# Optimization experiments

Hardware: AMD Instinct MI355X
Metric: run time of the kernel (lower is better)

## Reference

```python
import jax, jax.numpy as jnp
import numpy as np

B, LH, HF = 65536, 128, 32
VC_MIN = 0.0


def _theta_init():
    # Deterministic parameter init, matching the torch constructor defaults.
    def spinv(x):
        return float(np.log(np.exp(max(x, 1e-4)) - 1.0 + 1e-6))
    vals = [
        0.0,                                  # alpha_raw: log(0.5/(1-0.5))
        float(np.log(np.exp(1.0) - 1.0 + 1e-6)),   # c_raw  (c_init=1.0)
        float(np.log(np.exp(0.1) - 1.0 + 1e-6)),   # kappa_raw (kappa_init=0.1)
        float(np.log(np.exp(0.15) - 1.0 + 1e-6)),  # vc_raw (vc_eff=0.15)
        -6.0,   # log_qx
        -6.0,   # log_qu
        -5.0,   # log_r
        0.0,    # log_q_scale
        -6.0,   # log_p0_xx
        -4.0,   # log_p0_uu
        spinv(0.1),   # a1_raw
        spinv(0.05),  # d1_raw
        spinv(0.5),   # d2_raw
        spinv(0.5),   # d3_raw
        0.0,    # b1
        0.0,    # b2
        0.1,    # beta
        float(np.arctanh(0.9)),  # rho_m_raw
        -4.0,   # log_qm
        -4.0,   # log_p0_mm
    ]
    return np.asarray(vals, dtype=np.float32)


def setup_inputs() -> dict:
    key = jax.random.key(0)
    k1, k2, k3, k4, k5 = jax.random.split(key, 5)
    return {
        "v_hist": jax.random.normal(k1, (B, LH), dtype=jnp.float32),
        "dt_hist": 0.01 + 0.1 * jax.random.uniform(k2, (B, LH), dtype=jnp.float32),
        "x_obs_hist": jax.random.normal(k3, (B, LH), dtype=jnp.float32),
        "v_fut": jax.random.normal(k4, (B, HF), dtype=jnp.float32),
        "dt_fut": 0.01 + 0.1 * jax.random.uniform(k5, (B, HF), dtype=jnp.float32),
        "theta": jnp.asarray(_theta_init()),
    }


def _forward(v_hist, dt_hist, x_obs_hist, v_fut, dt_fut, theta):
    sp = jax.nn.softplus
    alpha = jax.nn.sigmoid(theta[0])
    c = sp(theta[1]); kappa = sp(theta[2]); vc = sp(theta[3]) + VC_MIN
    qx = jnp.exp(theta[4]); qu = jnp.exp(theta[5]); R = jnp.exp(theta[6])
    qs = jnp.exp(theta[7]); p0xx = jnp.exp(theta[8]); p0uu = jnp.exp(theta[9])
    a1 = sp(theta[10]); d1 = sp(theta[11]); d2 = sp(theta[12]); d3 = sp(theta[13])
    b1 = theta[14]; b2 = theta[15]; beta = theta[16]
    rho_m = jnp.tanh(theta[17]); qm = jnp.exp(theta[18]); p0mm = jnp.exp(theta[19])

    Bn, Lh = v_hist.shape
    dtype = v_hist.dtype
    eye = jnp.eye(3, dtype=dtype)

    def predict(s, P, v, dv, dt):
        x, u, m = s[:, 0], s[:, 1], s[:, 2]
        rho = jnp.exp(-alpha * dt)
        forcing = jax.nn.relu(v * v - vc * vc)
        cl = (-a1 * u + b1 * v + b2 * dv
              - d1 * u * u - d2 * u * jnp.abs(v) - d3 * u * jnp.abs(u))
        x_p = x + u * dt
        u_p = rho * u - kappa * x * dt + c * forcing * dt + cl * dt + beta * m
        m_p = rho_m * m
        s_p = jnp.stack([x_p, u_p, m_p], axis=1)
        z = jnp.zeros_like(dt); o = jnp.ones_like(dt)
        Fm = jnp.stack([
            jnp.stack([o, dt, z], axis=1),
            jnp.stack([-kappa * dt, rho, beta * o], axis=1),
            jnp.stack([z, z, rho_m * o], axis=1)], axis=1)  # [B,3,3]
        qdiag = jnp.stack([qs * qx * dt, qs * qu * dt, qm * o], axis=1)  # [B,3]
        P_p = jnp.einsum('bij,bjk,blk->bil', Fm, P, Fm) + qdiag[:, :, None] * eye
        return s_p, P_p

    def update(s, P, y):
        innov = y - s[:, 0]
        S = P[:, 0, 0] + R
        K = P[:, :, 0] / S[:, None]            # [B,3]
        s_u = s + K * innov[:, None]
        IKH = eye - K[:, :, None] * eye[0]     # I - K H, H = [1,0,0]
        P_u = (jnp.einsum('bij,bjk,blk->bil', IKH, P, IKH)
               + R * (K[:, :, None] * K[:, None, :]))
        return s_u, P_u

    s0 = jnp.zeros((Bn, 3), dtype).at[:, 0].set(x_obs_hist[:, 0])
    P0 = jnp.broadcast_to(jnp.diag(jnp.stack([p0xx, p0uu, p0mm])).astype(dtype),
                          (Bn, 3, 3))

    # History steps k = 1 .. Lh-1 (scan over time axis, [T, B] layout)
    v_h = v_hist[:, :Lh - 1].T
    dv_h = jnp.concatenate(
        [jnp.zeros((1, Bn), dtype), (v_hist[:, 1:Lh - 1] - v_hist[:, :Lh - 2]).T], axis=0)
    dt_h = jnp.maximum(dt_hist[:, 1:], 1e-6).T
    y_h = x_obs_hist[:, 1:].T

    def hist_step(carry, inp):
        s, P = carry
        v, dv, dt, y = inp
        s, P = predict(s, P, v, dv, dt)
        s, P = update(s, P, y)
        return (s, P), None

    (s, P), _ = jax.lax.scan(hist_step, (s0, P0), (v_h, dv_h, dt_h, y_h))

    # Future rollout (predict only)
    v_f = v_fut.T
    dv_f = (v_fut - jnp.concatenate([v_hist[:, -1:], v_fut[:, :-1]], axis=1)).T
    dt_f = jnp.maximum(dt_fut, 1e-6).T

    def fut_step(carry, inp):
        s, P = carry
        v, dv, dt = inp
        s, P = predict(s, P, v, dv, dt)
        return (s, P), (s[:, 0], P[:, 0, 0], s[:, 1])

    _, (x_preds, x_vars, u_ests) = jax.lax.scan(fut_step, (s, P), (v_f, dv_f, dt_f))
    return x_preds.T, x_vars.T, u_ests.T  # each [B, Hf]


def reference(v_hist, dt_hist, x_obs_hist, v_fut, dt_fut, theta):
    return _forward(v_hist, dt_hist, x_obs_hist, v_fut, dt_fut, theta)
```

## Files before the change

kernel.cpp:

```cpp
#include <hip/hip_runtime.h>
#include <math.h>

#define BATCH 65536
#define LHIST 128
#define HFUT  32

__device__ __forceinline__ float softplusf(float x) {
    return fmaxf(x, 0.0f) + log1pf(expf(-fabsf(x)));
}

__global__ __launch_bounds__(256, 1) void kalman_fwd(
    const float* __restrict__ v_hist,
    const float* __restrict__ dt_hist,
    const float* __restrict__ x_obs,
    const float* __restrict__ v_fut,
    const float* __restrict__ dt_fut,
    const float* __restrict__ theta,
    float* __restrict__ out)
{
    const int b = blockIdx.x * 256 + threadIdx.x;

    const float alpha = 1.0f / (1.0f + expf(-theta[0]));
    const float c     = softplusf(theta[1]);
    const float kappa = softplusf(theta[2]);
    const float vc    = softplusf(theta[3]);
    const float qx    = expf(theta[4]);
    const float qu    = expf(theta[5]);
    const float Rn    = expf(theta[6]);
    const float qs    = expf(theta[7]);
    const float p0xx  = expf(theta[8]);
    const float p0uu  = expf(theta[9]);
    const float a1    = softplusf(theta[10]);
    const float d1    = softplusf(theta[11]);
    const float d2    = softplusf(theta[12]);
    const float d3    = softplusf(theta[13]);
    const float b1    = theta[14];
    const float b2    = theta[15];
    const float beta  = theta[16];
    const float rho_m = tanhf(theta[17]);
    const float qm    = expf(theta[18]);
    const float p0mm  = expf(theta[19]);
    const float vc2   = vc * vc;
    const float qxs   = qs * qx;
    const float qus   = qs * qu;
    const float nal2e = -alpha * 1.44269504088896340736f;

    float sx = 0.0f, su = 0.0f, sm = 0.0f;
    float p00 = p0xx, p01 = 0.0f, p02 = 0.0f, p11 = p0uu, p12 = 0.0f, p22 = p0mm;

    auto predict = [&](float v, float dv, float dt_raw) {
        float dt  = fmaxf(dt_raw, 1e-6f);
        float rho = __builtin_amdgcn_exp2f(nal2e * dt);
        float forcing = fmaxf(v * v - vc2, 0.0f);
        float cl = -a1 * su + b1 * v + b2 * dv
                 - d1 * su * su - d2 * su * fabsf(v) - d3 * su * fabsf(su);
        float kdt = kappa * dt;
        float x_p = sx + su * dt;
        float u_p = rho * su - kdt * sx + c * forcing * dt + cl * dt + beta * sm;
        float m_p = rho_m * sm;
        float f0 = p00 + dt * p01;
        float f1 = p01 + dt * p11;
        float f2 = p02 + dt * p12;
        float g0 = -kdt * p00 + rho * p01 + beta * p02;
        float g1 = -kdt * p01 + rho * p11 + beta * p12;
        float g2 = -kdt * p02 + rho * p12 + beta * p22;
        float n00 = f0 + dt * f1 + qxs * dt;
        float n01 = -kdt * f0 + rho * f1 + beta * f2;
        float n02 = rho_m * f2;
        float n11 = -kdt * g0 + rho * g1 + beta * g2 + qus * dt;
        float n12 = rho_m * g2;
        float n22 = rho_m * rho_m * p22 + qm;
        sx = x_p; su = u_p; sm = m_p;
        p00 = n00; p01 = n01; p02 = n02; p11 = n11; p12 = n12; p22 = n22;
    };

    auto update = [&](float y) {
        float innov = y - sx;
        float S    = p00 + Rn;
        float Sinv = __builtin_amdgcn_rcpf(S);
        float K0 = p00 * Sinv, K1 = p01 * Sinv, K2 = p02 * Sinv;
        sx += K0 * innov; su += K1 * innov; sm += K2 * innov;
        float a = 1.0f - K0;
        float n00 = a * a * p00 + Rn * K0 * K0;
        float n01 = a * (p01 - K1 * p00) + Rn * K0 * K1;
        float n02 = a * (p02 - K2 * p00) + Rn * K0 * K2;
        float n11 = S * K1 * K1 - 2.0f * K1 * p01 + p11;
        float n12 = S * K1 * K2 - K2 * p01 - K1 * p02 + p12;
        float n22 = S * K2 * K2 - 2.0f * K2 * p02 + p22;
        p00 = n00; p01 = n01; p02 = n02; p11 = n11; p12 = n12; p22 = n22;
    };

    const float4* v4 = (const float4*)(v_hist  + (size_t)b * LHIST);
    const float4* d4 = (const float4*)(dt_hist + (size_t)b * LHIST);
    const float4* y4 = (const float4*)(x_obs   + (size_t)b * LHIST);

    float4 AV0, AV1, AV2, AV3, AD0, AD1, AD2, AD3, AY0, AY1, AY2, AY3;
    float4 BV0, BV1, BV2, BV3, BD0, BD1, BD2, BD3, BY0, BY1, BY2, BY3;
    float vp1 = 0.0f, vp2 = 0.0f;

#define LOAD_CHUNK(k, P) do {                                                    \
    P##V0 = v4[4*(k)+0]; P##V1 = v4[4*(k)+1];                                    \
    P##V2 = v4[4*(k)+2]; P##V3 = v4[4*(k)+3];                                    \
    P##D0 = d4[4*(k)+0]; P##D1 = d4[4*(k)+1];                                    \
    P##D2 = d4[4*(k)+2]; P##D3 = d4[4*(k)+3];                                    \
    P##Y0 = y4[4*(k)+0]; P##Y1 = y4[4*(k)+1];                                    \
    P##Y2 = y4[4*(k)+2]; P##Y3 = y4[4*(k)+3];                                    \
} while (0)

#define KSTEP(vc_, vpv_, dtn_, yn_) do { predict((vc_), (vc_) - (vpv_), (dtn_)); update(yn_); } while (0)

#define CHUNK_TAIL(P) do {                                                       \
    KSTEP(P##V0.y, P##V0.x, P##D0.z, P##Y0.z);                                   \
    KSTEP(P##V0.z, P##V0.y, P##D0.w, P##Y0.w);                                   \
    KSTEP(P##V0.w, P##V0.z, P##D1.x, P##Y1.x);                                   \
    KSTEP(P##V1.x, P##V0.w, P##D1.y, P##Y1.y);                                   \
    KSTEP(P##V1.y, P##V1.x, P##D1.z, P##Y1.z);                                   \
    KSTEP(P##V1.z, P##V1.y, P##D1.w, P##Y1.w);                                   \
    KSTEP(P##V1.w, P##V1.z, P##D2.x, P##Y2.x);                                   \
    KSTEP(P##V2.x, P##V1.w, P##D2.y, P##Y2.y);                                   \
    KSTEP(P##V2.y, P##V2.x, P##D2.z, P##Y2.z);                                   \
    KSTEP(P##V2.z, P##V2.y, P##D2.w, P##Y2.w);                                   \
    KSTEP(P##V2.w, P##V2.z, P##D3.x, P##Y3.x);                                   \
    KSTEP(P##V3.x, P##V2.w, P##D3.y, P##Y3.y);                                   \
    KSTEP(P##V3.y, P##V3.x, P##D3.z, P##Y3.z);                                   \
    KSTEP(P##V3.z, P##V3.y, P##D3.w, P##Y3.w);                                   \
    vp2 = P##V3.z; vp1 = P##V3.w;                                                \
} while (0)

#define CHUNK(P) do {                                                            \
    predict(vp1, vp1 - vp2, P##D0.x);   update(P##Y0.x);                         \
    KSTEP(P##V0.x, vp1, P##D0.y, P##Y0.y);                                       \
    CHUNK_TAIL(P);                                                               \
} while (0)

    LOAD_CHUNK(0, A);
    LOAD_CHUNK(1, B);

    sx = AY0.x;
    predict(AV0.x, 0.0f, AD0.y); update(AY0.y);
    CHUNK_TAIL(A);

    #pragma unroll 1
    for (int k = 1; k <= 3; ++k) {
        LOAD_CHUNK(2 * k, A);
        CHUNK(B);
        LOAD_CHUNK(2 * k + 1, B);
        CHUNK(A);
    }

    const float4* vf4 = (const float4*)(v_fut  + (size_t)b * HFUT);
    const float4* df4 = (const float4*)(dt_fut + (size_t)b * HFUT);
    float4 VF0 = vf4[0], VF1 = vf4[1], VF2 = vf4[2], VF3 = vf4[3],
           VF4 = vf4[4], VF5 = vf4[5], VF6 = vf4[6], VF7 = vf4[7];
    float4 DF0 = df4[0], DF1 = df4[1], DF2 = df4[2], DF3 = df4[3],
           DF4 = df4[4], DF5 = df4[5], DF6 = df4[6], DF7 = df4[7];

    CHUNK(B);

    float4 OP0, OP1, OP2, OP3, OP4, OP5, OP6, OP7;
    float4 OV0, OV1, OV2, OV3, OV4, OV5, OV6, OV7;
    float4 OU0, OU1, OU2, OU3, OU4, OU5, OU6, OU7;
    float vp = vp1;

#define FUTQ(VF, DF, OP, OV, OU) do {                                            \
    predict(VF.x, VF.x - vp,   DF.x); OP.x = sx; OV.x = p00; OU.x = su;          \
    predict(VF.y, VF.y - VF.x, DF.y); OP.y = sx; OV.y = p00; OU.y = su;          \
    predict(VF.z, VF.z - VF.y, DF.z); OP.z = sx; OV.z = p00; OU.z = su;          \
    predict(VF.w, VF.w - VF.z, DF.w); OP.w = sx; OV.w = p00; OU.w = su;          \
    vp = VF.w;                                                                   \
} while (0)

    FUTQ(VF0, DF0, OP0, OV0, OU0);
    FUTQ(VF1, DF1, OP1, OV1, OU1);
    FUTQ(VF2, DF2, OP2, OV2, OU2);
    FUTQ(VF3, DF3, OP3, OV3, OU3);
    FUTQ(VF4, DF4, OP4, OV4, OU4);
    FUTQ(VF5, DF5, OP5, OV5, OU5);
    FUTQ(VF6, DF6, OP6, OV6, OU6);
    FUTQ(VF7, DF7, OP7, OV7, OU7);

    float4* xp = (float4*)(out + (size_t)b * HFUT);
    float4* xv = (float4*)(out + (size_t)BATCH * HFUT + (size_t)b * HFUT);
    float4* ue = (float4*)(out + 2 * (size_t)BATCH * HFUT + (size_t)b * HFUT);
    xp[0] = OP0; xp[1] = OP1; xp[2] = OP2; xp[3] = OP3;
    xp[4] = OP4; xp[5] = OP5; xp[6] = OP6; xp[7] = OP7;
    xv[0] = OV0; xv[1] = OV1; xv[2] = OV2; xv[3] = OV3;
    xv[4] = OV4; xv[5] = OV5; xv[6] = OV6; xv[7] = OV7;
    ue[0] = OU0; ue[1] = OU1; ue[2] = OU2; ue[3] = OU3;
    ue[4] = OU4; ue[5] = OU5; ue[6] = OU6; ue[7] = OU7;
}

extern "C" void kernel_launch(void* const* d_in, const int* in_sizes, int n_in,
                              void* d_out, int out_size, void* d_ws, size_t ws_size,
                              hipStream_t stream) {
    const float* v_hist  = (const float*)d_in[0];
    const float* dt_hist = (const float*)d_in[1];
    const float* x_obs   = (const float*)d_in[2];
    const float* v_fut   = (const float*)d_in[3];
    const float* dt_fut  = (const float*)d_in[4];
    const float* theta   = (const float*)d_in[5];
    float* out = (float*)d_out;

    dim3 grid(BATCH / 256), block(256);
    hipLaunchKernelGGL(kalman_fwd, grid, block, 0, stream,
                       v_hist, dt_hist, x_obs, v_fut, dt_fut, theta, out);
}
```

Before: 167.6 us.

## Simplify Kalman covariance update, use explicit FMAs, shrink prefetch chunks with sched barriers

The Joseph-form covariance update is replaced by the standard P - K*P' form, which needs far fewer multiplies per step. The predict math is rewritten as explicit fmaf chains. The history prefetch is cut from 16-step to 8-step double-buffered chunks, and sched_barrier calls keep loads from being reordered around the compute, which lowers register pressure. The simpler update form is less numerically robust, and the smaller chunks expose more load latency.

```diff
diff --git a/kernel.cpp b/kernel.cpp
--- a/kernel.cpp
+++ b/kernel.cpp
@@ -43,6 +43,7 @@
     const float vc2   = vc * vc;
     const float qxs   = qs * qx;
     const float qus   = qs * qu;
+    const float rm2   = rho_m * rho_m;
     const float nal2e = -alpha * 1.44269504088896340736f;
 
     float sx = 0.0f, su = 0.0f, sm = 0.0f;
@@ -51,25 +52,26 @@
     auto predict = [&](float v, float dv, float dt_raw) {
         float dt  = fmaxf(dt_raw, 1e-6f);
         float rho = __builtin_amdgcn_exp2f(nal2e * dt);
-        float forcing = fmaxf(v * v - vc2, 0.0f);
+        float forcing = fmaxf(fmaf(v, v, -vc2), 0.0f);
         float cl = -a1 * su + b1 * v + b2 * dv
                  - d1 * su * su - d2 * su * fabsf(v) - d3 * su * fabsf(su);
         float kdt = kappa * dt;
-        float x_p = sx + su * dt;
-        float u_p = rho * su - kdt * sx + c * forcing * dt + cl * dt + beta * sm;
+        float x_p = fmaf(su, dt, sx);
+        float u_p = fmaf(dt, fmaf(c, forcing, cl),
+                         fmaf(-kdt, sx, fmaf(rho, su, beta * sm)));
         float m_p = rho_m * sm;
-        float f0 = p00 + dt * p01;
-        float f1 = p01 + dt * p11;
-        float f2 = p02 + dt * p12;
-        float g0 = -kdt * p00 + rho * p01 + beta * p02;
-        float g1 = -kdt * p01 + rho * p11 + beta * p12;
-        float g2 = -kdt * p02 + rho * p12 + beta * p22;
-        float n00 = f0 + dt * f1 + qxs * dt;
-        float n01 = -kdt * f0 + rho * f1 + beta * f2;
+        float f0 = fmaf(dt, p01, p00);
+        float f1 = fmaf(dt, p11, p01);
+        float f2 = fmaf(dt, p12, p02);
+        float g0 = fmaf(-kdt, p00, fmaf(rho, p01, beta * p02));
+        float g1 = fmaf(-kdt, p01, fmaf(rho, p11, beta * p12));
+        float g2 = fmaf(-kdt, p02, fmaf(rho, p12, beta * p22));
+        float n00 = fmaf(dt, f1, f0) + qxs * dt;
+        float n01 = fmaf(-kdt, f0, fmaf(rho, f1, beta * f2));
         float n02 = rho_m * f2;
-        float n11 = -kdt * g0 + rho * g1 + beta * g2 + qus * dt;
+        float n11 = fmaf(-kdt, g0, fmaf(rho, g1, beta * g2)) + qus * dt;
         float n12 = rho_m * g2;
-        float n22 = rho_m * rho_m * p22 + qm;
+        float n22 = fmaf(rm2, p22, qm);
         sx = x_p; su = u_p; sm = m_p;
         p00 = n00; p01 = n01; p02 = n02; p11 = n11; p12 = n12; p22 = n22;
     };
@@ -79,73 +81,65 @@
         float S    = p00 + Rn;
         float Sinv = __builtin_amdgcn_rcpf(S);
         float K0 = p00 * Sinv, K1 = p01 * Sinv, K2 = p02 * Sinv;
-        sx += K0 * innov; su += K1 * innov; sm += K2 * innov;
+        sx = fmaf(K0, innov, sx);
+        su = fmaf(K1, innov, su);
+        sm = fmaf(K2, innov, sm);
+        float n11 = fmaf(-K1, p01, p11);
+        float n12 = fmaf(-K1, p02, p12);
+        float n22 = fmaf(-K2, p02, p22);
         float a = 1.0f - K0;
-        float n00 = a * a * p00 + Rn * K0 * K0;
-        float n01 = a * (p01 - K1 * p00) + Rn * K0 * K1;
-        float n02 = a * (p02 - K2 * p00) + Rn * K0 * K2;
-        float n11 = S * K1 * K1 - 2.0f * K1 * p01 + p11;
-        float n12 = S * K1 * K2 - K2 * p01 - K1 * p02 + p12;
-        float n22 = S * K2 * K2 - 2.0f * K2 * p02 + p22;
-        p00 = n00; p01 = n01; p02 = n02; p11 = n11; p12 = n12; p22 = n22;
+        p00 *= a; p01 *= a; p02 *= a;
+        p11 = n11; p12 = n12; p22 = n22;
     };
 
     const float4* v4 = (const float4*)(v_hist  + (size_t)b * LHIST);
     const float4* d4 = (const float4*)(dt_hist + (size_t)b * LHIST);
     const float4* y4 = (const float4*)(x_obs   + (size_t)b * LHIST);
 
-    float4 AV0, AV1, AV2, AV3, AD0, AD1, AD2, AD3, AY0, AY1, AY2, AY3;
-    float4 BV0, BV1, BV2, BV3, BD0, BD1, BD2, BD3, BY0, BY1, BY2, BY3;
+    float4 AV0, AV1, AD0, AD1, AY0, AY1;
+    float4 BV0, BV1, BD0, BD1, BY0, BY1;
     float vp1 = 0.0f, vp2 = 0.0f;
 
-#define LOAD_CHUNK(k, P) do {                                                    \
-    P##V0 = v4[4*(k)+0]; P##V1 = v4[4*(k)+1];                                    \
-    P##V2 = v4[4*(k)+2]; P##V3 = v4[4*(k)+3];                                    \
-    P##D0 = d4[4*(k)+0]; P##D1 = d4[4*(k)+1];                                    \
-    P##D2 = d4[4*(k)+2]; P##D3 = d4[4*(k)+3];                                    \
-    P##Y0 = y4[4*(k)+0]; P##Y1 = y4[4*(k)+1];                                    \
-    P##Y2 = y4[4*(k)+2]; P##Y3 = y4[4*(k)+3];                                    \
-} while (0)
+#define LOAD8(k, P) do {                                                        \
+    P##V0 = v4[2*(k)];   P##V1 = v4[2*(k)+1];                                   \
+    P##D0 = d4[2*(k)];   P##D1 = d4[2*(k)+1];                                   \
+    P##Y0 = y4[2*(k)];   P##Y1 = y4[2*(k)+1];                                   \
+} while (0)
+
+#define PINV() __builtin_amdgcn_sched_barrier(0x0006)
 
 #define KSTEP(vc_, vpv_, dtn_, yn_) do { predict((vc_), (vc_) - (vpv_), (dtn_)); update(yn_); } while (0)
 
-#define CHUNK_TAIL(P) do {                                                       \
-    KSTEP(P##V0.y, P##V0.x, P##D0.z, P##Y0.z);                                   \
-    KSTEP(P##V0.z, P##V0.y, P##D0.w, P##Y0.w);                                   \
-    KSTEP(P##V0.w, P##V0.z, P##D1.x, P##Y1.x);                                   \
-    KSTEP(P##V1.x, P##V0.w, P##D1.y, P##Y1.y);                                   \
-    KSTEP(P##V1.y, P##V1.x, P##D1.z, P##Y1.z);                                   \
-    KSTEP(P##V1.z, P##V1.y, P##D1.w, P##Y1.w);                                   \
-    KSTEP(P##V1.w, P##V1.z, P##D2.x, P##Y2.x);                                   \
-    KSTEP(P##V2.x, P##V1.w, P##D2.y, P##Y2.y);                                   \
-    KSTEP(P##V2.y, P##V2.x, P##D2.z, P##Y2.z);                                   \
-    KSTEP(P##V2.z, P##V2.y, P##D2.w, P##Y2.w);                                   \
-    KSTEP(P##V2.w, P##V2.z, P##D3.x, P##Y3.x);                                   \
-    KSTEP(P##V3.x, P##V2.w, P##D3.y, P##Y3.y);                                   \
-    KSTEP(P##V3.y, P##V3.x, P##D3.z, P##Y3.z);                                   \
-    KSTEP(P##V3.z, P##V3.y, P##D3.w, P##Y3.w);                                   \
-    vp2 = P##V3.z; vp1 = P##V3.w;                                                \
-} while (0)
-
-#define CHUNK(P) do {                                                            \
-    predict(vp1, vp1 - vp2, P##D0.x);   update(P##Y0.x);                         \
-    KSTEP(P##V0.x, vp1, P##D0.y, P##Y0.y);                                       \
-    CHUNK_TAIL(P);                                                               \
-} while (0)
-
-    LOAD_CHUNK(0, A);
-    LOAD_CHUNK(1, B);
+#define CHUNK8_TAIL(P) do {                                                     \
+    KSTEP(P##V0.y, P##V0.x, P##D0.z, P##Y0.z);                                  \
+    KSTEP(P##V0.z, P##V0.y, P##D0.w, P##Y0.w);                                  \
+    KSTEP(P##V0.w, P##V0.z, P##D1.x, P##Y1.x);                                  \
+    KSTEP(P##V1.x, P##V0.w, P##D1.y, P##Y1.y);                                  \
+    KSTEP(P##V1.y, P##V1.x, P##D1.z, P##Y1.z);                                  \
+    KSTEP(P##V1.z, P##V1.y, P##D1.w, P##Y1.w);                                  \
+    vp2 = P##V1.z; vp1 = P##V1.w;                                               \
+} while (0)
+
+#define CHUNK8(P) do {                                                          \
+    predict(vp1, vp1 - vp2, P##D0.x);  update(P##Y0.x);           \
+    KSTEP(P##V0.x, vp1, P##D0.y, P##Y0.y);                        \
+    CHUNK8_TAIL(P);                                                             \
+} while (0)
+
+    LOAD8(0, A);
+    LOAD8(1, B);
+    PINV();
 
     sx = AY0.x;
     predict(AV0.x, 0.0f, AD0.y); update(AY0.y);
-    CHUNK_TAIL(A);
+    CHUNK8_TAIL(A);
 
     #pragma unroll 1
-    for (int k = 1; k <= 3; ++k) {
-        LOAD_CHUNK(2 * k, A);
-        CHUNK(B);
-        LOAD_CHUNK(2 * k + 1, B);
-        CHUNK(A);
+    for (int i = 1; i <= 13; i += 2) {
+        LOAD8(i + 1, A);  PINV();
+        CHUNK8(B);
+        LOAD8(i + 2, B);  PINV();
+        CHUNK8(A);
     }
 
     const float4* vf4 = (const float4*)(v_fut  + (size_t)b * HFUT);
@@ -154,20 +148,21 @@
            VF4 = vf4[4], VF5 = vf4[5], VF6 = vf4[6], VF7 = vf4[7];
     float4 DF0 = df4[0], DF1 = df4[1], DF2 = df4[2], DF3 = df4[3],
            DF4 = df4[4], DF5 = df4[5], DF6 = df4[6], DF7 = df4[7];
-
-    CHUNK(B);
+    PINV();
+
+    CHUNK8(B);
 
     float4 OP0, OP1, OP2, OP3, OP4, OP5, OP6, OP7;
     float4 OV0, OV1, OV2, OV3, OV4, OV5, OV6, OV7;
     float4 OU0, OU1, OU2, OU3, OU4, OU5, OU6, OU7;
     float vp = vp1;
 
-#define FUTQ(VF, DF, OP, OV, OU) do {                                            \
-    predict(VF.x, VF.x - vp,   DF.x); OP.x = sx; OV.x = p00; OU.x = su;          \
-    predict(VF.y, VF.y - VF.x, DF.y); OP.y = sx; OV.y = p00; OU.y = su;          \
-    predict(VF.z, VF.z - VF.y, DF.z); OP.z = sx; OV.z = p00; OU.z = su;          \
-    predict(VF.w, VF.w - VF.z, DF.w); OP.w = sx; OV.w = p00; OU.w = su;          \
-    vp = VF.w;                                                                   \
+#define FUTQ(VF, DF, OP, OV, OU) do {                                           \
+    predict(VF.x, VF.x - vp,   DF.x); OP.x = sx; OV.x = p00; OU.x = su;         \
+    predict(VF.y, VF.y - VF.x, DF.y); OP.y = sx; OV.y = p00; OU.y = su;         \
+    predict(VF.z, VF.z - VF.y, DF.z); OP.z = sx; OV.z = p00; OU.z = su;         \
+    predict(VF.w, VF.w - VF.z, DF.w); OP.w = sx; OV.w = p00; OU.w = su;         \
+    vp = VF.w;                                                                  \
 } while (0)
 
     FUTQ(VF0, DF0, OP0, OV0, OU0);
```

After: 162.3 us. 1.03x faster.
